# Kernel tuning notes

Measured on AMD Instinct MI355X. Metric: run time of the kernel, lower is better.

Reference implementation:

```python
import jax, jax.numpy as jnp
import numpy as np

GRID_SIZE = 5
SPLINE_ORDER = 3
GRID_RANGE = (-1.0, 1.0)


def b_splines(x, grid, spline_order=SPLINE_ORDER):
    # x: [B, in], grid: [G] with G = grid_size + 2*spline_order + 1
    x = x[..., None]                      # [B, in, 1]
    g = grid[None, None, :]               # [1, 1, G]
    bases = ((x >= g[..., :-1]) & (x < g[..., 1:])).astype(x.dtype)  # [B, in, G-1]
    for k in range(1, spline_order + 1):
        left = (x - g[..., :-(k + 1)]) / (g[..., k:-1] - g[..., :-(k + 1)]) * bases[..., :-1]
        right = (g[..., k + 1:] - x) / (g[..., k + 1:] - g[..., 1:-k]) * bases[..., 1:]
        bases = left + right
    return bases                          # [B, in, grid_size + spline_order]


def setup_inputs() -> dict:
    key = jax.random.key(0)
    k1, k2, k3, k4 = jax.random.split(key, 4)
    B, IN, OUT = 32768, 256, 256
    n_coef = GRID_SIZE + SPLINE_ORDER  # 8
    h = (GRID_RANGE[1] - GRID_RANGE[0]) / GRID_SIZE
    grid = jnp.arange(-SPLINE_ORDER, GRID_SIZE + SPLINE_ORDER + 1, dtype=jnp.float32) * h + GRID_RANGE[0]  # [12]
    x = jax.random.normal(k1, (B, IN), dtype=jnp.float32)
    base_weight = jax.random.normal(k2, (OUT, IN), dtype=jnp.float32) * np.sqrt(2.0 / IN)
    spline_weight = jax.random.normal(k3, (OUT, IN, n_coef), dtype=jnp.float32) * (0.1 / GRID_SIZE)
    spline_scaler = jax.random.normal(k4, (OUT, IN), dtype=jnp.float32) * np.sqrt(2.0 / IN)
    return {"x": x, "base_weight": base_weight, "spline_weight": spline_weight,
            "spline_scaler": spline_scaler, "grid": grid}


def reference(x, base_weight, spline_weight, spline_scaler, grid):
    B = x.shape[0]
    out_features = base_weight.shape[0]
    # base branch: silu(x) @ base_weight^T
    base_out = jnp.matmul(jax.nn.silu(x), base_weight.T)  # [B, out]
    # spline branch
    bases = b_splines(x, grid)                             # [B, in, n_coef]
    scaled_w = spline_weight * spline_scaler[..., None]    # [out, in, n_coef]
    spline_out = jnp.matmul(bases.reshape(B, -1), scaled_w.reshape(out_features, -1).T)
    return base_out + spline_out
```

## Files before the change

### kernel.cpp

```cpp
#include <hip/hip_runtime.h>
#include <hip/hip_bf16.h>
#include <stdint.h>


#define IN_F 256
#define OUT_F 256
#define KDIM 2304
#define BK 64
#define NCHUNK (KDIM / BK)
#define WC_BYTES ((size_t)OUT_F * KDIM * 2)

#define AS1 __attribute__((address_space(1)))
#define AS3 __attribute__((address_space(3)))

typedef float f32x4 __attribute__((ext_vector_type(4)));
typedef short bf16x8 __attribute__((ext_vector_type(8)));

__device__ __forceinline__ uint32_t f2bf(float f) {
    union { float f; uint32_t u; } c; c.f = f;
    uint32_t u = c.u;
    return (u + 0x7FFFu + ((u >> 16) & 1u)) >> 16;
}

__device__ __forceinline__ float silu_f(float v) {
    return v / (1.0f + __expf(-v));
}

__global__ void build_w(const float* __restrict__ bw, const float* __restrict__ sw,
                        const float* __restrict__ ss, unsigned short* __restrict__ Wc) {
    const int o = blockIdx.x;
    const int i = threadIdx.x;
    Wc[o * KDIM + i] = (unsigned short)f2bf(bw[o * IN_F + i]);
    const float scal = ss[o * IN_F + i];
    const float4* swv = reinterpret_cast<const float4*>(sw + (size_t)(o * IN_F + i) * 8);
    float4 s0 = swv[0], s1 = swv[1];
    uint4 wv;
    wv.x = f2bf(s0.x * scal) | (f2bf(s0.y * scal) << 16);
    wv.y = f2bf(s0.z * scal) | (f2bf(s0.w * scal) << 16);
    wv.z = f2bf(s1.x * scal) | (f2bf(s1.y * scal) << 16);
    wv.w = f2bf(s1.z * scal) | (f2bf(s1.w * scal) << 16);
    *reinterpret_cast<uint4*>(Wc + o * KDIM + IN_F + i * 8) = wv;
}

__launch_bounds__(512, 2)
__global__ void kan_fused(const float* __restrict__ x, const unsigned short* __restrict__ Wc,
                          float* __restrict__ out) {
    __shared__ __align__(16) unsigned short As0[128 * 64];
    __shared__ __align__(16) unsigned short As1[128 * 64];
    __shared__ __align__(16) unsigned short Bs0[256 * 64];
    __shared__ __align__(16) unsigned short Bs1[256 * 64];

    const int row0 = blockIdx.x * 128;
    const int tid = threadIdx.x;
    const int lane = tid & 63;
    const int w = tid >> 6;
    const int wm = w >> 2;
    const int wn = w & 3;
    const int l15 = lane & 15;
    const int q = lane >> 4;

    const int sr = lane >> 3;
    const int s  = lane & 7;
    const int g  = s ^ sr;
    const int srow = w * 16 + sr;

    const int brow = w * 32 + sr;

    const float* xs0 = x + (size_t)(row0 + srow) * IN_F + g * 8;
    const float* xs1 = xs0 + 8 * IN_F;

    f32x4 acc[4][4] = {};
    float xr[2][8];
    uint64_t pk2[2];
    int j02[2];

    auto stage_b = [&](int kc, unsigned short* Bsb) {
#pragma unroll
        for (int j = 0; j < 4; ++j) {
            const unsigned short* gp =
                Wc + (size_t)(brow + j * 8) * KDIM + kc * BK + g * 8;
            __builtin_amdgcn_global_load_lds((const AS1 void*)gp,
                                             (AS3 void*)&Bsb[(w * 32 + j * 8) * 64],
                                             16, 0, 0);
        }
    };
    auto load_x = [&](int kc) {
        if (kc < 4) {
            const float* p0 = xs0 + kc * 64;
            const float* p1 = xs1 + kc * 64;
            float4 a0 = *reinterpret_cast<const float4*>(p0);
            float4 b0 = *reinterpret_cast<const float4*>(p0 + 4);
            float4 a1 = *reinterpret_cast<const float4*>(p1);
            float4 b1 = *reinterpret_cast<const float4*>(p1 + 4);
            xr[0][0] = a0.x; xr[0][1] = a0.y; xr[0][2] = a0.z; xr[0][3] = a0.w;
            xr[0][4] = b0.x; xr[0][5] = b0.y; xr[0][6] = b0.z; xr[0][7] = b0.w;
            xr[1][0] = a1.x; xr[1][1] = a1.y; xr[1][2] = a1.z; xr[1][3] = a1.w;
            xr[1][4] = b1.x; xr[1][5] = b1.y; xr[1][6] = b1.z; xr[1][7] = b1.w;
        } else {
            const int i0 = (kc - 4) * 8 + g;
            float xx0 = xs0[i0 - g * 8];
            float xx1 = xs1[i0 - g * 8];
#pragma unroll
            for (int j = 0; j < 2; ++j) {
                float xx = j ? xx1 : xx0;
                float u = __builtin_fmaf(xx, 2.5f, 5.5f);
                float jf = floorf(u);
                float t = u - jf;
                j02[j] = (int)jf;
                float t2 = t * t, t3 = t2 * t;
                float p3 = t3 * (1.0f / 6.0f);
                float p2 = -0.5f * t3 + 0.5f * t2 + 0.5f * t + (1.0f / 6.0f);
                float p1 = 0.5f * t3 - t2 + (2.0f / 3.0f);
                float omt = 1.0f - t;
                float p0 = omt * omt * omt * (1.0f / 6.0f);
                pk2[j] = (uint64_t)f2bf(p0) | ((uint64_t)f2bf(p1) << 16) |
                         ((uint64_t)f2bf(p2) << 32) | ((uint64_t)f2bf(p3) << 48);
            }
        }
    };
    auto write_a = [&](int kc, unsigned short* Asb) {
        if (kc < 4) {
#pragma unroll
            for (int j = 0; j < 2; ++j) {
                uint4 wv;
                wv.x = f2bf(silu_f(xr[j][0])) | (f2bf(silu_f(xr[j][1])) << 16);
                wv.y = f2bf(silu_f(xr[j][2])) | (f2bf(silu_f(xr[j][3])) << 16);
                wv.z = f2bf(silu_f(xr[j][4])) | (f2bf(silu_f(xr[j][5])) << 16);
                wv.w = f2bf(silu_f(xr[j][6])) | (f2bf(silu_f(xr[j][7])) << 16);
                *reinterpret_cast<uint4*>(&Asb[(srow + j * 8) * 64 + s * 8]) = wv;
            }
        } else {
#pragma unroll
            for (int j = 0; j < 2; ++j) {
                int j0 = j02[j];
                uint64_t pk = ((unsigned)j0 <= 10u) ? pk2[j] : 0ull;
                int jc = j0 < 0 ? 0 : (j0 > 10 ? 10 : j0);
                int sh = jc * 16 - 48;
                unsigned __int128 v = (unsigned __int128)pk;
                v = (sh >= 0) ? (v << sh) : (v >> (-sh));
                uint4 wv;
                wv.x = (uint32_t)v;
                wv.y = (uint32_t)(v >> 32);
                wv.z = (uint32_t)(v >> 64);
                wv.w = (uint32_t)(v >> 96);
                *reinterpret_cast<uint4*>(&Asb[(srow + j * 8) * 64 + s * 8]) = wv;
            }
        }
    };
    auto mfma_chunk = [&](const unsigned short* Asb, const unsigned short* Bsb) {
#pragma unroll
        for (int ks = 0; ks < 2; ++ks) {
            const int g0 = ks * 4 + q;
            bf16x8 af[4], bfv[4];
#pragma unroll
            for (int mt = 0; mt < 4; ++mt) {
                int r = wm * 64 + mt * 16 + l15;
                af[mt] = *reinterpret_cast<const bf16x8*>(
                    &Asb[r * 64 + ((g0 ^ (r & 7)) << 3)]);
            }
#pragma unroll
            for (int nt = 0; nt < 4; ++nt) {
                int r = wn * 64 + nt * 16 + l15;
                bfv[nt] = *reinterpret_cast<const bf16x8*>(
                    &Bsb[r * 64 + ((g0 ^ (r & 7)) << 3)]);
            }
#pragma unroll
            for (int mt = 0; mt < 4; ++mt)
#pragma unroll
                for (int nt = 0; nt < 4; ++nt)
                    acc[mt][nt] = __builtin_amdgcn_mfma_f32_16x16x32_bf16(
                        af[mt], bfv[nt], acc[mt][nt], 0, 0, 0);
        }
    };

#define CHUNK_STEP(KC, ASC, BSC, ASN, BSN)            \
    {                                                 \
        if ((KC) + 1 < NCHUNK) {                      \
            stage_b((KC) + 1, BSN);                   \
            load_x((KC) + 1);                         \
        }                                             \
        mfma_chunk(ASC, BSC);                         \
        if ((KC) + 1 < NCHUNK) write_a((KC) + 1, ASN);\
        __syncthreads();                              \
    }

    stage_b(0, Bs0);
    load_x(0);
    write_a(0, As0);
    __syncthreads();

#pragma unroll 1
    for (int it = 0; it < NCHUNK / 2; ++it) {
        const int kc0 = it * 2;
        CHUNK_STEP(kc0,     As0, Bs0, As1, Bs1)
        CHUNK_STEP(kc0 + 1, As1, Bs1, As0, Bs0)
    }

    float* outp = out + (size_t)(row0 + wm * 64 + q * 4) * OUT_F + wn * 64 + l15;
#pragma unroll
    for (int mt = 0; mt < 4; ++mt) {
#pragma unroll
        for (int nt = 0; nt < 4; ++nt) {
#pragma unroll
            for (int r = 0; r < 4; ++r)
                outp[(size_t)(mt * 16 + r) * OUT_F + nt * 16] = acc[mt][nt][r];
        }
    }
}

extern "C" void kernel_launch(void* const* d_in, const int* in_sizes, int n_in,
                              void* d_out, int out_size, void* d_ws, size_t ws_size,
                              hipStream_t stream) {
    const float* x  = (const float*)d_in[0];
    const float* bw = (const float*)d_in[1];
    const float* sw = (const float*)d_in[2];
    const float* ss = (const float*)d_in[3];
    unsigned short* Wc = (unsigned short*)d_ws;

    build_w<<<dim3(OUT_F), dim3(IN_F), 0, stream>>>(bw, sw, ss, Wc);

    const int B_ROWS = in_sizes[0] / IN_F;
    kan_fused<<<dim3(B_ROWS / 128), dim3(512), 0, stream>>>(x, Wc, (float*)d_out);
}
```

Before: 150.2 us.

## Build A fragments in registers, drop A LDS staging, shrink block tile

The activation tile no longer goes through shared memory. Each wave computes its B-spline basis and SiLU MFMA A-fragments directly in registers from x and feeds them to the MFMAs, with the spline chunks reordered ahead of the base chunks. The block shrinks to 64 rows and 4 waves, and each wave now covers 32x128 instead of 64x64. This removes the LDS writes, reads and bank traffic for A, but each wave sees fewer rows per B fragment load, so B LDS reads per MFMA rise and the SiLU path does uncached-looking global loads inside the compute loop.

```diff
diff --git a/kernel.cpp b/kernel.cpp
--- a/kernel.cpp
+++ b/kernel.cpp
@@ -7,7 +7,7 @@
 #define OUT_F 256
 #define KDIM 2304
 #define BK 64
-#define NCHUNK (KDIM / BK)
+#define NCHUNK 36
 #define WC_BYTES ((size_t)OUT_F * KDIM * 2)
 
 #define AS1 __attribute__((address_space(1)))
@@ -15,6 +15,8 @@
 
 typedef float f32x4 __attribute__((ext_vector_type(4)));
 typedef short bf16x8 __attribute__((ext_vector_type(8)));
+
+union U4B8 { uint4 u; bf16x8 v; };
 
 __device__ __forceinline__ uint32_t f2bf(float f) {
     union { float f; uint32_t u; } c; c.f = f;
@@ -24,6 +26,43 @@
 
 __device__ __forceinline__ float silu_f(float v) {
     return v / (1.0f + __expf(-v));
+}
+
+__device__ __forceinline__ bf16x8 basis_frag(float xx) {
+    float u = __builtin_fmaf(xx, 2.5f, 5.5f);
+    float jf = floorf(u);
+    float t = u - jf;
+    int j0 = (int)jf;
+    float t2 = t * t, t3 = t2 * t;
+    float p3 = t3 * (1.0f / 6.0f);
+    float p2 = -0.5f * t3 + 0.5f * t2 + 0.5f * t + (1.0f / 6.0f);
+    float p1 = 0.5f * t3 - t2 + (2.0f / 3.0f);
+    float omt = 1.0f - t;
+    float p0 = omt * omt * omt * (1.0f / 6.0f);
+    uint64_t pk = (uint64_t)f2bf(p0) | ((uint64_t)f2bf(p1) << 16) |
+                  ((uint64_t)f2bf(p2) << 32) | ((uint64_t)f2bf(p3) << 48);
+    if ((unsigned)j0 > 10u) pk = 0ull;
+    int jc = j0 < 0 ? 0 : (j0 > 10 ? 10 : j0);
+    int sh = jc * 16 - 48;
+    unsigned __int128 v = (unsigned __int128)pk;
+    v = (sh >= 0) ? (v << sh) : (v >> (-sh));
+    U4B8 r;
+    r.u.x = (uint32_t)v;
+    r.u.y = (uint32_t)(v >> 32);
+    r.u.z = (uint32_t)(v >> 64);
+    r.u.w = (uint32_t)(v >> 96);
+    return r.v;
+}
+
+__device__ __forceinline__ bf16x8 silu_frag(const float* p) {
+    float4 a = *reinterpret_cast<const float4*>(p);
+    float4 b = *reinterpret_cast<const float4*>(p + 4);
+    U4B8 r;
+    r.u.x = f2bf(silu_f(a.x)) | (f2bf(silu_f(a.y)) << 16);
+    r.u.y = f2bf(silu_f(a.z)) | (f2bf(silu_f(a.w)) << 16);
+    r.u.z = f2bf(silu_f(b.x)) | (f2bf(silu_f(b.y)) << 16);
+    r.u.w = f2bf(silu_f(b.z)) | (f2bf(silu_f(b.w)) << 16);
+    return r.v;
 }
 
 __global__ void build_w(const float* __restrict__ bw, const float* __restrict__ sw,
@@ -42,168 +81,106 @@
     *reinterpret_cast<uint4*>(Wc + o * KDIM + IN_F + i * 8) = wv;
 }
 
-__launch_bounds__(512, 2)
+__launch_bounds__(256, 2)
 __global__ void kan_fused(const float* __restrict__ x, const unsigned short* __restrict__ Wc,
                           float* __restrict__ out) {
-    __shared__ __align__(16) unsigned short As0[128 * 64];
-    __shared__ __align__(16) unsigned short As1[128 * 64];
     __shared__ __align__(16) unsigned short Bs0[256 * 64];
     __shared__ __align__(16) unsigned short Bs1[256 * 64];
 
-    const int row0 = blockIdx.x * 128;
+    const int row0 = blockIdx.x * 64;
     const int tid = threadIdx.x;
     const int lane = tid & 63;
     const int w = tid >> 6;
-    const int wm = w >> 2;
-    const int wn = w & 3;
+    const int wm = w >> 1;
+    const int wn = w & 1;
     const int l15 = lane & 15;
     const int q = lane >> 4;
 
     const int sr = lane >> 3;
     const int s  = lane & 7;
     const int g  = s ^ sr;
-    const int srow = w * 16 + sr;
-
-    const int brow = w * 32 + sr;
-
-    const float* xs0 = x + (size_t)(row0 + srow) * IN_F + g * 8;
-    const float* xs1 = xs0 + 8 * IN_F;
-
-    f32x4 acc[4][4] = {};
-    float xr[2][8];
-    uint64_t pk2[2];
-    int j02[2];
-
-    auto stage_b = [&](int kc, unsigned short* Bsb) {
-#pragma unroll
-        for (int j = 0; j < 4; ++j) {
-            const unsigned short* gp =
-                Wc + (size_t)(brow + j * 8) * KDIM + kc * BK + g * 8;
-            __builtin_amdgcn_global_load_lds((const AS1 void*)gp,
-                                             (AS3 void*)&Bsb[(w * 32 + j * 8) * 64],
+    const int brow = w * 64 + sr;
+
+    const float* xrow0 = x + (size_t)(row0 + wm * 32 + l15) * IN_F;
+    const float* xrow1 = xrow0 + 16 * IN_F;
+
+    f32x4 acc[2][8] = {};
+    float xA[4], xB[4];
+
+    auto stage_b = [&](int c, unsigned short* Bsb) {
+        const int colbase = (c < 32) ? (256 + c * 64) : ((c - 32) * 64);
+        const unsigned short* src = Wc + (size_t)brow * KDIM + colbase + g * 8;
+#pragma unroll
+        for (int j = 0; j < 8; ++j) {
+            __builtin_amdgcn_global_load_lds((const AS1 void*)(src + (size_t)j * 8 * KDIM),
+                                             (AS3 void*)&Bsb[(w * 64 + j * 8) * 64],
                                              16, 0, 0);
         }
     };
-    auto load_x = [&](int kc) {
-        if (kc < 4) {
-            const float* p0 = xs0 + kc * 64;
-            const float* p1 = xs1 + kc * 64;
-            float4 a0 = *reinterpret_cast<const float4*>(p0);
-            float4 b0 = *reinterpret_cast<const float4*>(p0 + 4);
-            float4 a1 = *reinterpret_cast<const float4*>(p1);
-            float4 b1 = *reinterpret_cast<const float4*>(p1 + 4);
-            xr[0][0] = a0.x; xr[0][1] = a0.y; xr[0][2] = a0.z; xr[0][3] = a0.w;
-            xr[0][4] = b0.x; xr[0][5] = b0.y; xr[0][6] = b0.z; xr[0][7] = b0.w;
-            xr[1][0] = a1.x; xr[1][1] = a1.y; xr[1][2] = a1.z; xr[1][3] = a1.w;
-            xr[1][4] = b1.x; xr[1][5] = b1.y; xr[1][6] = b1.z; xr[1][7] = b1.w;
-        } else {
-            const int i0 = (kc - 4) * 8 + g;
-            float xx0 = xs0[i0 - g * 8];
-            float xx1 = xs1[i0 - g * 8];
-#pragma unroll
-            for (int j = 0; j < 2; ++j) {
-                float xx = j ? xx1 : xx0;
-                float u = __builtin_fmaf(xx, 2.5f, 5.5f);
-                float jf = floorf(u);
-                float t = u - jf;
-                j02[j] = (int)jf;
-                float t2 = t * t, t3 = t2 * t;
-                float p3 = t3 * (1.0f / 6.0f);
-                float p2 = -0.5f * t3 + 0.5f * t2 + 0.5f * t + (1.0f / 6.0f);
-                float p1 = 0.5f * t3 - t2 + (2.0f / 3.0f);
-                float omt = 1.0f - t;
-                float p0 = omt * omt * omt * (1.0f / 6.0f);
-                pk2[j] = (uint64_t)f2bf(p0) | ((uint64_t)f2bf(p1) << 16) |
-                         ((uint64_t)f2bf(p2) << 32) | ((uint64_t)f2bf(p3) << 48);
+    auto prefetch_x = [&](int c, float* xs) {
+        const int i0 = c * 8 + q;
+        xs[0] = xrow0[i0];
+        xs[1] = xrow0[i0 + 4];
+        xs[2] = xrow1[i0];
+        xs[3] = xrow1[i0 + 4];
+    };
+    auto do_chunk = [&](int c, const unsigned short* Bsb, const float* xs) {
+#pragma unroll
+        for (int ks = 0; ks < 2; ++ks) {
+            bf16x8 af0, af1;
+            if (c < 32) {
+                af0 = basis_frag(xs[ks]);
+                af1 = basis_frag(xs[2 + ks]);
+            } else {
+                const int off = (c - 32) * 64 + ks * 32 + q * 8;
+                af0 = silu_frag(xrow0 + off);
+                af1 = silu_frag(xrow1 + off);
             }
-        }
-    };
-    auto write_a = [&](int kc, unsigned short* Asb) {
-        if (kc < 4) {
-#pragma unroll
-            for (int j = 0; j < 2; ++j) {
-                uint4 wv;
-                wv.x = f2bf(silu_f(xr[j][0])) | (f2bf(silu_f(xr[j][1])) << 16);
-                wv.y = f2bf(silu_f(xr[j][2])) | (f2bf(silu_f(xr[j][3])) << 16);
-                wv.z = f2bf(silu_f(xr[j][4])) | (f2bf(silu_f(xr[j][5])) << 16);
-                wv.w = f2bf(silu_f(xr[j][6])) | (f2bf(silu_f(xr[j][7])) << 16);
-                *reinterpret_cast<uint4*>(&Asb[(srow + j * 8) * 64 + s * 8]) = wv;
-            }
-        } else {
-#pragma unroll
-            for (int j = 0; j < 2; ++j) {
-                int j0 = j02[j];
-                uint64_t pk = ((unsigned)j0 <= 10u) ? pk2[j] : 0ull;
-                int jc = j0 < 0 ? 0 : (j0 > 10 ? 10 : j0);
-                int sh = jc * 16 - 48;
-                unsigned __int128 v = (unsigned __int128)pk;
-                v = (sh >= 0) ? (v << sh) : (v >> (-sh));
-                uint4 wv;
-                wv.x = (uint32_t)v;
-                wv.y = (uint32_t)(v >> 32);
-                wv.z = (uint32_t)(v >> 64);
-                wv.w = (uint32_t)(v >> 96);
-                *reinterpret_cast<uint4*>(&Asb[(srow + j * 8) * 64 + s * 8]) = wv;
-            }
-        }
-    };
-    auto mfma_chunk = [&](const unsigned short* Asb, const unsigned short* Bsb) {
-#pragma unroll
-        for (int ks = 0; ks < 2; ++ks) {
             const int g0 = ks * 4 + q;
-            bf16x8 af[4], bfv[4];
-#pragma unroll
-            for (int mt = 0; mt < 4; ++mt) {
-                int r = wm * 64 + mt * 16 + l15;
-                af[mt] = *reinterpret_cast<const bf16x8*>(
-                    &Asb[r * 64 + ((g0 ^ (r & 7)) << 3)]);
-            }
-#pragma unroll
-            for (int nt = 0; nt < 4; ++nt) {
-                int r = wn * 64 + nt * 16 + l15;
+            bf16x8 bfv[8];
+#pragma unroll
+            for (int nt = 0; nt < 8; ++nt) {
+                int r = wn * 128 + nt * 16 + l15;
                 bfv[nt] = *reinterpret_cast<const bf16x8*>(
                     &Bsb[r * 64 + ((g0 ^ (r & 7)) << 3)]);
             }
 #pragma unroll
-            for (int mt = 0; mt < 4; ++mt)
-#pragma unroll
-                for (int nt = 0; nt < 4; ++nt)
-                    acc[mt][nt] = __builtin_amdgcn_mfma_f32_16x16x32_bf16(
-                        af[mt], bfv[nt], acc[mt][nt], 0, 0, 0);
+            for (int nt = 0; nt < 8; ++nt) {
+                acc[0][nt] = __builtin_amdgcn_mfma_f32_16x16x32_bf16(af0, bfv[nt], acc[0][nt], 0, 0, 0);
+                acc[1][nt] = __builtin_amdgcn_mfma_f32_16x16x32_bf16(af1, bfv[nt], acc[1][nt], 0, 0, 0);
+            }
         }
     };
 
-#define CHUNK_STEP(KC, ASC, BSC, ASN, BSN)            \
-    {                                                 \
-        if ((KC) + 1 < NCHUNK) {                      \
-            stage_b((KC) + 1, BSN);                   \
-            load_x((KC) + 1);                         \
-        }                                             \
-        mfma_chunk(ASC, BSC);                         \
-        if ((KC) + 1 < NCHUNK) write_a((KC) + 1, ASN);\
-        __syncthreads();                              \
-    }
-
     stage_b(0, Bs0);
-    load_x(0);
-    write_a(0, As0);
+    prefetch_x(0, xA);
     __syncthreads();
 
 #pragma unroll 1
     for (int it = 0; it < NCHUNK / 2; ++it) {
-        const int kc0 = it * 2;
-        CHUNK_STEP(kc0,     As0, Bs0, As1, Bs1)
-        CHUNK_STEP(kc0 + 1, As1, Bs1, As0, Bs0)
+        const int c0 = it * 2;
+        if (c0 + 1 < NCHUNK) {
+            stage_b(c0 + 1, Bs1);
+            if (c0 + 1 < 32) prefetch_x(c0 + 1, xB);
+        }
+        do_chunk(c0, Bs0, xA);
+        __syncthreads();
+        if (c0 + 2 < NCHUNK) {
+            stage_b(c0 + 2, Bs0);
+            if (c0 + 2 < 32) prefetch_x(c0 + 2, xA);
+        }
+        do_chunk(c0 + 1, Bs1, xB);
+        __syncthreads();
     }
 
-    float* outp = out + (size_t)(row0 + wm * 64 + q * 4) * OUT_F + wn * 64 + l15;
-#pragma unroll
-    for (int mt = 0; mt < 4; ++mt) {
-#pragma unroll
-        for (int nt = 0; nt < 4; ++nt) {
+    float* outp = out + (size_t)(row0 + wm * 32 + q * 4) * OUT_F + wn * 128 + l15;
+#pragma unroll
+    for (int rg = 0; rg < 2; ++rg) {
+#pragma unroll
+        for (int nt = 0; nt < 8; ++nt) {
 #pragma unroll
             for (int r = 0; r < 4; ++r)
-                outp[(size_t)(mt * 16 + r) * OUT_F + nt * 16] = acc[mt][nt][r];
+                outp[(size_t)(rg * 16 + r) * OUT_F + nt * 16] = acc[rg][nt][r];
         }
     }
 }
@@ -220,5 +197,5 @@
     build_w<<<dim3(OUT_F), dim3(IN_F), 0, stream>>>(bw, sw, ss, Wc);
 
     const int B_ROWS = in_sizes[0] / IN_F;
-    kan_fused<<<dim3(B_ROWS / 128), dim3(512), 0, stream>>>(x, Wc, (float*)d_out);
-}
+    kan_fused<<<dim3(B_ROWS / 64), dim3(256), 0, stream>>>(x, Wc, (float*)d_out);
+}
```

Measured after the change: 153.1 us. No clear change (+1.9%).
